# Optimization experiments

Measured on AMD Instinct MI355X. Metric: run time of the kernel, lower is better.

## Reference

```python
import jax, jax.numpy as jnp
import numpy as np

N_NODES = 100000
N_EDGES = 1600000
FEAT = 64
HEADS = 8
OUT_C = 8  # per-head out channels; HEADS*OUT_C == FEAT
BATCH = 64
MAXLEN = 2048
NEG_SLOPE = 0.2  # PyG GATConv default


def setup_inputs() -> dict:
    key = jax.random.key(0)
    ks = jax.random.split(key, 8)
    x = jax.random.normal(ks[0], (N_NODES, FEAT), dtype=jnp.float32)
    edge_index = jax.random.randint(ks[1], (2, N_EDGES), 0, N_NODES, dtype=jnp.int64)
    traj_seqs = jax.random.randint(ks[2], (BATCH, MAXLEN), 0, N_NODES, dtype=jnp.int64)
    seq_lengths = jax.random.randint(ks[3], (BATCH,), 1, MAXLEN, dtype=jnp.int64)
    # GATConv parameters (glorot-ish init)
    W = jax.random.normal(ks[4], (FEAT, HEADS * OUT_C), dtype=jnp.float32) * (1.0 / np.sqrt(FEAT))
    att_src = jax.random.normal(ks[5], (HEADS, OUT_C), dtype=jnp.float32) * 0.1
    att_dst = jax.random.normal(ks[6], (HEADS, OUT_C), dtype=jnp.float32) * 0.1
    bias = jnp.zeros((HEADS * OUT_C,), dtype=jnp.float32)
    return {"x": x, "W": W, "att_src": att_src, "att_dst": att_dst, "bias": bias,
            "edge_index": edge_index, "traj_seqs": traj_seqs, "seq_lengths": seq_lengths}


def reference(x, W, att_src, att_dst, bias, edge_index, traj_seqs, seq_lengths):
    N = x.shape[0]
    # PyG GATConv adds self loops by default
    loop = jnp.arange(N, dtype=edge_index.dtype)
    src = jnp.concatenate([edge_index[0], loop])  # message source j
    dst = jnp.concatenate([edge_index[1], loop])  # message target i

    xw = (x @ W).reshape(N, HEADS, OUT_C)              # [N,H,C]
    a_src = jnp.sum(xw * att_src, axis=-1)             # [N,H]
    a_dst = jnp.sum(xw * att_dst, axis=-1)             # [N,H]

    # edge attention logits and segment softmax over incoming edges of dst
    e = jax.nn.leaky_relu(a_src[src] + a_dst[dst], NEG_SLOPE)   # [E,H]
    m = jax.ops.segment_max(e, dst, num_segments=N)             # [N,H]
    m = jnp.where(jnp.isfinite(m), m, 0.0)
    ex = jnp.exp(e - m[dst])
    denom = jax.ops.segment_sum(ex, dst, num_segments=N)        # [N,H] (>0 via self loops)
    alpha = ex / denom[dst]                                     # [E,H]

    msg = alpha[:, :, None] * xw[src]                           # [E,H,C]
    out = jax.ops.segment_sum(msg, dst, num_segments=N)         # [N,H,C]
    node_emb = jax.nn.relu(out.reshape(N, HEADS * OUT_C) + bias)

    # batched gather into padded [B, maxlen, F] tensor, zero past seq_lengths
    emb = node_emb[traj_seqs]                                   # [B,L,F]
    mask = jnp.arange(traj_seqs.shape[1])[None, :] < seq_lengths[:, None]
    emb = emb * mask[:, :, None].astype(emb.dtype)
    return emb, seq_lengths
```

## Files before the change

### kernel.cpp

```cpp
#include <hip/hip_runtime.h>
#include <hip/hip_bf16.h>
#include <hip/hip_fp8.h>
#include <hip/hip_fp16.h>

#define N_NODESC 100000
#define N_EDGESC 1600000
#define FEATC 64
#define HEADSC 8
#define BATCHC 64
#define MAXLENC 2048
#define NBUCK 500
#define BSZ 200
#define HSZ 100
#define CAPH 3072
#define P3_EDGES 8192
#define K1B 782
#define HCHUNK 16
#define K2B 98

typedef float f32x2 __attribute__((ext_vector_type(2)));

__device__ __forceinline__ float b2f(unsigned short u){
  union { unsigned u; float f; } c; c.u = ((unsigned)u) << 16; return c.f;
}
__device__ __forceinline__ unsigned short f2b(float f){
  union { float f; unsigned u; } c; c.f = f;
  unsigned r = c.u + 0x7fffu + ((c.u >> 16) & 1u);
  return (unsigned short)(r >> 16);
}
__device__ __forceinline__ int clampi(int v, int lo, int hi){
  return v < lo ? lo : (v > hi ? hi : v);
}
__device__ __forceinline__ void unpack8(uint4 v, float* o){
  o[0] = b2f((unsigned short)(v.x & 0xffff)); o[1] = b2f((unsigned short)(v.x >> 16));
  o[2] = b2f((unsigned short)(v.y & 0xffff)); o[3] = b2f((unsigned short)(v.y >> 16));
  o[4] = b2f((unsigned short)(v.z & 0xffff)); o[5] = b2f((unsigned short)(v.z >> 16));
  o[6] = b2f((unsigned short)(v.w & 0xffff)); o[7] = b2f((unsigned short)(v.w >> 16));
}
__device__ __forceinline__ void cvt4(unsigned v, float* o){
  f32x2 lo = __builtin_amdgcn_cvt_pk_f32_fp8((int)v, false);
  f32x2 hi = __builtin_amdgcn_cvt_pk_f32_fp8((int)v, true);
  o[0] = lo.x; o[1] = lo.y; o[2] = hi.x; o[3] = hi.y;
}

__global__ __launch_bounds__(256) void k_pre(
    const unsigned short* __restrict__ x, const unsigned short* __restrict__ W,
    const unsigned short* __restrict__ attS, const unsigned short* __restrict__ attD,
    const int* __restrict__ ei,
    unsigned char* __restrict__ xw8, __half* __restrict__ a_srch,
    float* __restrict__ a_dst, int* __restrict__ cc)
{
  __shared__ unsigned short Wh[64 * 64];
  __shared__ float as_s[64];
  __shared__ float ad_s[64];
  __shared__ uint4 xs_s[128 * 9];
  __shared__ int hh[NBUCK];
  int t = threadIdx.x;

  if (blockIdx.x >= K1B) {
    for (int i = t; i < NBUCK; i += 256) hh[i] = 0;
    __syncthreads();
    int base4 = (blockIdx.x - K1B) * (HCHUNK * 256);
    #pragma unroll 4
    for (int it = 0; it < HCHUNK; it++) {
      int g = base4 + it * 256 + t;
      if (g < N_EDGESC / 4) {
        int4 d = ((const int4*)(ei + N_EDGESC))[g];
        atomicAdd(&hh[clampi(d.x, 0, N_NODESC - 1) / BSZ], 1);
        atomicAdd(&hh[clampi(d.y, 0, N_NODESC - 1) / BSZ], 1);
        atomicAdd(&hh[clampi(d.z, 0, N_NODESC - 1) / BSZ], 1);
        atomicAdd(&hh[clampi(d.w, 0, N_NODESC - 1) / BSZ], 1);
      }
    }
    __syncthreads();
    for (int i = t; i < NBUCK; i += 256) if (hh[i]) atomicAdd(&cc[i], hh[i]);
    return;
  }

  {
    const uint4* W4 = (const uint4*)W;
    ((uint4*)Wh)[t]       = W4[t];
    ((uint4*)Wh)[t + 256] = W4[t + 256];
  }
  if (t < 64) { as_s[t] = b2f(attS[t]); ad_s[t] = b2f(attD[t]); }
  {
    const uint4* x4 = (const uint4*)x;
    int gbase = blockIdx.x * 1024;
    #pragma unroll
    for (int r = 0; r < 4; r++) {
      int idx = t + r * 256;
      int nl = idx >> 3, i = idx & 7;
      uint4 v = make_uint4(0u, 0u, 0u, 0u);
      int gi = gbase + idx;
      if (gi < N_NODESC * 8) v = x4[gi];
      xs_s[nl * 9 + i] = v;
    }
  }
  __syncthreads();

  int g    = t & 3;
  int slot = t >> 2;
  int ln0  = slot * 2;
  int n0   = blockIdx.x * 128 + ln0;

  float acc[2][16];
  #pragma unroll
  for (int j = 0; j < 2; j++)
    #pragma unroll
    for (int c = 0; c < 16; c++) acc[j][c] = 0.f;

  const uint4* Wq = (const uint4*)Wh;
  for (int i = 0; i < 8; i++) {
    float xu[2][8];
    #pragma unroll
    for (int j = 0; j < 2; j++) unpack8(xs_s[(ln0 + j) * 9 + i], xu[j]);
    #pragma unroll
    for (int u = 0; u < 8; u++) {
      int k = i * 8 + u;
      float wf[16];
      unpack8(Wq[k * 8 + g * 2 + 0], wf);
      unpack8(Wq[k * 8 + g * 2 + 1], wf + 8);
      #pragma unroll
      for (int j = 0; j < 2; j++) {
        float xk = xu[j][u];
        #pragma unroll
        for (int c = 0; c < 16; c++) acc[j][c] += xk * wf[c];
      }
    }
  }

  #pragma unroll
  for (int j = 0; j < 2; j++) {
    int n = n0 + j;
    if (n >= N_NODESC) break;
    union { unsigned u[4]; unsigned char b[16]; } pk;
    #pragma unroll
    for (int c = 0; c < 16; c++)
      pk.b[c] = (unsigned char)__hip_fp8_e4m3(acc[j][c]).__x;
    uint4 o; o.x = pk.u[0]; o.y = pk.u[1]; o.z = pk.u[2]; o.w = pk.u[3];
    *((uint4*)(xw8 + (size_t)n * 64 + g * 16)) = o;

    #pragma unroll
    for (int hl = 0; hl < 2; hl++) {
      int h = g * 2 + hl;
      float sa = 0.f, sd = 0.f;
      #pragma unroll
      for (int c = 0; c < 8; c++) {
        sa += acc[j][hl * 8 + c] * as_s[h * 8 + c];
        sd += acc[j][hl * 8 + c] * ad_s[h * 8 + c];
      }
      a_srch[n * 8 + h] = __float2half(sa);
      a_dst[n * 8 + h] = sd;
    }
  }
}

__global__ __launch_bounds__(1024) void k_csort(const int* __restrict__ ei,
                                                const int* __restrict__ cc,
                                                int* __restrict__ gcur,
                                                unsigned* __restrict__ cs,
                                                int* __restrict__ boff) {
  __shared__ int bst[512];
  __shared__ int h[NBUCK], lst[NBUCK], lcur[NBUCK], gb[NBUCK];
  __shared__ int sc[512];
  __shared__ unsigned sorted[P3_EDGES];
  __shared__ unsigned short sbk[P3_EDGES];
  int t = threadIdx.x;
  int base = blockIdx.x * P3_EDGES;
  for (int i = t; i < NBUCK; i += 1024) h[i] = 0;
  int myc = 0;
  if (t < 512) { myc = (t < NBUCK) ? cc[t] : 0; bst[t] = myc; }
  __syncthreads();
  for (int off = 1; off < 512; off <<= 1) {
    int v = 0;
    if (t < 512) { v = bst[t]; if (t >= off) v += bst[t - off]; }
    __syncthreads();
    if (t < 512) bst[t] = v;
    __syncthreads();
  }
  if (blockIdx.x == 0 && t < NBUCK) boff[t] = bst[t] - myc;
  unsigned pk[8]; int bk[8];
  #pragma unroll
  for (int k = 0; k < 8; k++) {
    int idx = base + k * 1024 + t;
    bk[k] = -1;
    if (idx < N_EDGESC) {
      int s = clampi(ei[idx], 0, N_NODESC - 1);
      int d = clampi(ei[N_EDGESC + idx], 0, N_NODESC - 1);
      int b = d / BSZ;
      pk[k] = (unsigned)s | ((unsigned)(d - b * BSZ) << 17);
      bk[k] = b;
      atomicAdd(&h[b], 1);
    }
  }
  __syncthreads();
  if (t < 512) sc[t] = (t < NBUCK) ? h[t] : 0;
  __syncthreads();
  for (int off = 1; off < 512; off <<= 1) {
    int v = 0;
    if (t < 512) { v = sc[t]; if (t >= off) v += sc[t - off]; }
    __syncthreads();
    if (t < 512) sc[t] = v;
    __syncthreads();
  }
  if (t < NBUCK) {
    int ex = sc[t] - h[t];
    lst[t] = ex; lcur[t] = ex;
    if (h[t]) gb[t] = (bst[t] - myc) + atomicAdd(&gcur[t], h[t]);
  }
  __syncthreads();
  #pragma unroll
  for (int k = 0; k < 8; k++) if (bk[k] >= 0) {
    int p = atomicAdd(&lcur[bk[k]], 1);
    sorted[p] = pk[k];
    sbk[p] = (unsigned short)bk[k];
  }
  __syncthreads();
  int cnt = N_EDGESC - base; if (cnt > P3_EDGES) cnt = P3_EDGES;
  #pragma unroll
  for (int k = 0; k < 8; k++) {
    int i = k * 1024 + t;
    if (i < cnt) {
      int b = sbk[i];
      cs[gb[b] + (i - lst[b])] = sorted[i];
    }
  }
}

__global__ __launch_bounds__(512) void k_aggf(
    const __half* __restrict__ a_srch, const float* __restrict__ a_dst,
    const unsigned char* __restrict__ xw8, const unsigned* __restrict__ cs,
    const int* __restrict__ cc, const int* __restrict__ boff,
    const unsigned short* __restrict__ bias, unsigned short* __restrict__ nembh)
{
  __shared__ int lcnt[128], loff[128], lcur[128];
  __shared__ int ssrc[CAPH];
  int t = threadIdx.x;
  int b = blockIdx.x >> 1;
  int dlo = (blockIdx.x & 1) * HSZ;
  int base = boff[b];
  int cnt  = cc[b];
  if (cnt > 12 * 512) cnt = 12 * 512;

  if (t < 128) lcnt[t] = 0;
  __syncthreads();

  unsigned ce[12];
  #pragma unroll
  for (int j = 0; j < 12; j++) {
    int i = t + j * 512;
    ce[j] = 0xFFFFFFFFu;
    if (i < cnt) {
      unsigned e = cs[base + i];
      int dl = (int)(e >> 17);
      if (dl >= dlo && dl < dlo + HSZ) {
        ce[j] = e;
        atomicAdd(&lcnt[dl - dlo], 1);
      }
    }
  }
  __syncthreads();
  if (t < 128) loff[t] = lcnt[t];
  __syncthreads();
  for (int off = 1; off < 128; off <<= 1) {
    int v = 0;
    if (t < 128) { v = loff[t]; if (t >= off) v += loff[t - off]; }
    __syncthreads();
    if (t < 128) loff[t] = v;
    __syncthreads();
  }
  if (t < 128) { int ex = loff[t] - lcnt[t]; loff[t] = ex; lcur[t] = ex; }
  __syncthreads();
  #pragma unroll
  for (int j = 0; j < 12; j++) if (ce[j] != 0xFFFFFFFFu) {
    int p = atomicAdd(&lcur[(int)(ce[j] >> 17) - dlo], 1);
    if (p < CAPH) ssrc[p] = (int)(ce[j] & 0x1FFFFu);
  }
  __syncthreads();

  int wv = t >> 6;
  int l  = t & 63;
  int s  = l >> 2;
  int q  = l & 3;
  int d2 = s * 8 + wv;

  if (d2 < HSZ) {
    int dst = b * BSZ + dlo + d2;

    float2 sa2 = __half22float2(*(const __half2*)(a_srch + dst * 8 + q * 2));
    float2 ad2 = *(const float2*)(a_dst + dst * 8 + q * 2);
    float z0 = sa2.x + ad2.x, z1 = sa2.y + ad2.y;
    float den0 = __expf(fmaxf(z0, 0.2f * z0));
    float den1 = __expf(fmaxf(z1, 0.2f * z1));

    uint4 xs = *(const uint4*)(xw8 + (size_t)dst * 64 + q * 16);
    float xv[16];
    cvt4(xs.x, xv); cvt4(xs.y, xv + 4); cvt4(xs.z, xv + 8); cvt4(xs.w, xv + 12);
    float acc[16];
    #pragma unroll
    for (int c = 0; c < 8; c++) { acc[c] = den0 * xv[c]; acc[8 + c] = den1 * xv[8 + c]; }

    int beg = loff[d2]; if (beg > CAPH) beg = CAPH;
    int end2 = beg + lcnt[d2]; if (end2 > CAPH) end2 = CAPH;

    int nA = (beg < end2) ? ssrc[beg] : 0;
    int nB = (beg + 1 < end2) ? ssrc[beg + 1] : 0;
    __half2 aA = *(const __half2*)(a_srch + nA * 8 + q * 2);
    uint4   xA = *(const uint4*)(xw8 + (size_t)nA * 64 + q * 16);
    __half2 aB = *(const __half2*)(a_srch + nB * 8 + q * 2);
    uint4   xB = *(const uint4*)(xw8 + (size_t)nB * 64 + q * 16);

    for (int i = beg; i < end2; i++) {
      float2 af = __half22float2(aA);
      uint4  xc = xA;
      aA = aB; xA = xB;
      int nn = (i + 2 < end2) ? ssrc[i + 2] : 0;
      aB = *(const __half2*)(a_srch + nn * 8 + q * 2);
      xB = *(const uint4*)(xw8 + (size_t)nn * 64 + q * 16);

      float e0 = af.x + ad2.x, e1 = af.y + ad2.y;
      float w0 = __expf(fmaxf(e0, 0.2f * e0));
      float w1 = __expf(fmaxf(e1, 0.2f * e1));
      den0 += w0; den1 += w1;
      float yv[16];
      cvt4(xc.x, yv); cvt4(xc.y, yv + 4); cvt4(xc.z, yv + 8); cvt4(xc.w, yv + 12);
      #pragma unroll
      for (int c = 0; c < 8; c++) { acc[c] += w0 * yv[c]; acc[8 + c] += w1 * yv[8 + c]; }
    }

    float inv0 = __builtin_amdgcn_rcpf(den0);
    float inv1 = __builtin_amdgcn_rcpf(den1);
    uint4 bb0 = ((const uint4*)bias)[q * 2];
    uint4 bb1 = ((const uint4*)bias)[q * 2 + 1];
    unsigned bw[8] = {bb0.x, bb0.y, bb0.z, bb0.w, bb1.x, bb1.y, bb1.z, bb1.w};
    unsigned ow[8];
    #pragma unroll
    for (int p = 0; p < 8; p++) {
      float inv = (p < 4) ? inv0 : inv1;
      float v0 = acc[p * 2]     * inv + b2f((unsigned short)(bw[p] & 0xffff));
      float v1 = acc[p * 2 + 1] * inv + b2f((unsigned short)(bw[p] >> 16));
      v0 = fmaxf(v0, 0.f); v1 = fmaxf(v1, 0.f);
      ow[p] = (unsigned)f2b(v0) | ((unsigned)f2b(v1) << 16);
    }
    uint4 o0 = make_uint4(ow[0], ow[1], ow[2], ow[3]);
    uint4 o1 = make_uint4(ow[4], ow[5], ow[6], ow[7]);
    ((uint4*)nembh)[(size_t)dst * 8 + q * 2]     = o0;
    ((uint4*)nembh)[(size_t)dst * 8 + q * 2 + 1] = o1;
  }
}

__global__ __launch_bounds__(256) void k6_gather(
    const unsigned short* __restrict__ nembh, const int* __restrict__ traj,
    const int* __restrict__ lens, float* __restrict__ out)
{
  int gid = blockIdx.x * 256 + threadIdx.x;
  if (gid < BATCHC * MAXLENC * 16) {
    int b = gid >> 15;
    int rem = gid & 32767;
    int l = rem >> 4;
    int ch = rem & 15;
    int len = clampi(lens[b], 0, MAXLENC);
    float4 val = make_float4(0.f, 0.f, 0.f, 0.f);
    if (l < len) {
      int node = clampi(traj[b * MAXLENC + l], 0, N_NODESC - 1);
      uint2 q = ((const uint2*)nembh)[(size_t)node * 16 + ch];
      val = make_float4(b2f((unsigned short)(q.x & 0xffff)),
                        b2f((unsigned short)(q.x >> 16)),
                        b2f((unsigned short)(q.y & 0xffff)),
                        b2f((unsigned short)(q.y >> 16)));
    }
    ((float4*)out)[gid] = val;
  }
  if (gid < BATCHC) {
    out[(size_t)BATCHC * MAXLENC * FEATC + gid] = (float)lens[gid];
  }
}

extern "C" void kernel_launch(void* const* d_in, const int* in_sizes, int n_in,
                              void* d_out, int out_size, void* d_ws, size_t ws_size,
                              hipStream_t stream) {
  const unsigned short* x    = (const unsigned short*)d_in[0];
  const unsigned short* W    = (const unsigned short*)d_in[1];
  const unsigned short* attS = (const unsigned short*)d_in[2];
  const unsigned short* attD = (const unsigned short*)d_in[3];
  const unsigned short* bias = (const unsigned short*)d_in[4];
  const int* ei   = (const int*)d_in[5];
  const int* traj = (const int*)d_in[6];
  const int* lens = (const int*)d_in[7];
  float* out = (float*)d_out;

  float* F = (float*)d_ws;
  unsigned char* xw8 = (unsigned char*)d_ws;
  __half* a_srch = (__half*)(F + 3200000);
  float* a_dst   = F + 4000000;
  int* ccounts   = (int*)(F + 4900000);
  int* gcur      = (int*)(F + 4900000) + 512;
  int* boff      = (int*)(F + 4900000) + 1024;
  unsigned* cs   = (unsigned*)(F + 5000000);
  unsigned short* nembh = (unsigned short*)(F + 6700000);

  hipMemsetAsync(ccounts, 0, 1024 * sizeof(int), stream);
  k_pre<<<K1B + K2B, 256, 0, stream>>>(
      x, W, attS, attD, ei, xw8, a_srch, a_dst, ccounts);
  k_csort<<<(N_EDGESC + P3_EDGES - 1) / P3_EDGES, 1024, 0, stream>>>(ei, ccounts, gcur, cs, boff);
  k_aggf<<<NBUCK * 2, 512, 0, stream>>>(a_srch, a_dst, xw8, cs, ccounts, boff, bias, nembh);
  k6_gather<<<(BATCHC * MAXLENC * 16 + 255) / 256, 256, 0, stream>>>(nembh, traj, lens, out);
}
```

Baseline: 171.4 us.

## Halve per-thread nodes in projection and scatter edges directly in bucket sort

```diff
diff --git a/kernel.cpp b/kernel.cpp
--- a/kernel.cpp
+++ b/kernel.cpp
@@ -13,10 +13,11 @@
 #define BSZ 200
 #define HSZ 100
 #define CAPH 3072
-#define P3_EDGES 8192
-#define K1B 782
+#define K1B 1563
 #define HCHUNK 16
 #define K2B 98
+#define CS_EPB 4096
+#define CSB 391
 
 typedef float f32x2 __attribute__((ext_vector_type(2)));
 
@@ -53,7 +54,7 @@
   __shared__ unsigned short Wh[64 * 64];
   __shared__ float as_s[64];
   __shared__ float ad_s[64];
-  __shared__ uint4 xs_s[128 * 9];
+  __shared__ uint4 xs_s[64 * 9];
   __shared__ int hh[NBUCK];
   int t = threadIdx.x;
 
@@ -85,9 +86,9 @@
   if (t < 64) { as_s[t] = b2f(attS[t]); ad_s[t] = b2f(attD[t]); }
   {
     const uint4* x4 = (const uint4*)x;
-    int gbase = blockIdx.x * 1024;
-    #pragma unroll
-    for (int r = 0; r < 4; r++) {
+    int gbase = blockIdx.x * 512;
+    #pragma unroll
+    for (int r = 0; r < 2; r++) {
       int idx = t + r * 256;
       int nl = idx >> 3, i = idx & 7;
       uint4 v = make_uint4(0u, 0u, 0u, 0u);
@@ -100,43 +101,33 @@
 
   int g    = t & 3;
   int slot = t >> 2;
-  int ln0  = slot * 2;
-  int n0   = blockIdx.x * 128 + ln0;
-
-  float acc[2][16];
-  #pragma unroll
-  for (int j = 0; j < 2; j++)
-    #pragma unroll
-    for (int c = 0; c < 16; c++) acc[j][c] = 0.f;
+  int n    = blockIdx.x * 64 + slot;
+
+  float acc[16];
+  #pragma unroll
+  for (int c = 0; c < 16; c++) acc[c] = 0.f;
 
   const uint4* Wq = (const uint4*)Wh;
   for (int i = 0; i < 8; i++) {
-    float xu[2][8];
-    #pragma unroll
-    for (int j = 0; j < 2; j++) unpack8(xs_s[(ln0 + j) * 9 + i], xu[j]);
+    float xu[8];
+    unpack8(xs_s[slot * 9 + i], xu);
     #pragma unroll
     for (int u = 0; u < 8; u++) {
       int k = i * 8 + u;
       float wf[16];
       unpack8(Wq[k * 8 + g * 2 + 0], wf);
       unpack8(Wq[k * 8 + g * 2 + 1], wf + 8);
+      float xk = xu[u];
       #pragma unroll
-      for (int j = 0; j < 2; j++) {
-        float xk = xu[j][u];
-        #pragma unroll
-        for (int c = 0; c < 16; c++) acc[j][c] += xk * wf[c];
-      }
-    }
-  }
-
-  #pragma unroll
-  for (int j = 0; j < 2; j++) {
-    int n = n0 + j;
-    if (n >= N_NODESC) break;
+      for (int c = 0; c < 16; c++) acc[c] += xk * wf[c];
+    }
+  }
+
+  if (n < N_NODESC) {
     union { unsigned u[4]; unsigned char b[16]; } pk;
     #pragma unroll
     for (int c = 0; c < 16; c++)
-      pk.b[c] = (unsigned char)__hip_fp8_e4m3(acc[j][c]).__x;
+      pk.b[c] = (unsigned char)__hip_fp8_e4m3(acc[c]).__x;
     uint4 o; o.x = pk.u[0]; o.y = pk.u[1]; o.z = pk.u[2]; o.w = pk.u[3];
     *((uint4*)(xw8 + (size_t)n * 64 + g * 16)) = o;
 
@@ -146,8 +137,8 @@
       float sa = 0.f, sd = 0.f;
       #pragma unroll
       for (int c = 0; c < 8; c++) {
-        sa += acc[j][hl * 8 + c] * as_s[h * 8 + c];
-        sd += acc[j][hl * 8 + c] * ad_s[h * 8 + c];
+        sa += acc[hl * 8 + c] * as_s[h * 8 + c];
+        sd += acc[hl * 8 + c] * ad_s[h * 8 + c];
       }
       a_srch[n * 8 + h] = __float2half(sa);
       a_dst[n * 8 + h] = sd;
@@ -155,34 +146,33 @@
   }
 }
 
-__global__ __launch_bounds__(1024) void k_csort(const int* __restrict__ ei,
-                                                const int* __restrict__ cc,
-                                                int* __restrict__ gcur,
-                                                unsigned* __restrict__ cs,
-                                                int* __restrict__ boff) {
+__global__ __launch_bounds__(512) void k_csort(const int* __restrict__ ei,
+                                               const int* __restrict__ cc,
+                                               int* __restrict__ gcur,
+                                               unsigned* __restrict__ cs,
+                                               int* __restrict__ boff) {
   __shared__ int bst[512];
-  __shared__ int h[NBUCK], lst[NBUCK], lcur[NBUCK], gb[NBUCK];
-  __shared__ int sc[512];
-  __shared__ unsigned sorted[P3_EDGES];
-  __shared__ unsigned short sbk[P3_EDGES];
+  __shared__ int h[NBUCK];
+  __shared__ int lcur[NBUCK];
   int t = threadIdx.x;
-  int base = blockIdx.x * P3_EDGES;
-  for (int i = t; i < NBUCK; i += 1024) h[i] = 0;
-  int myc = 0;
-  if (t < 512) { myc = (t < NBUCK) ? cc[t] : 0; bst[t] = myc; }
+  int base = blockIdx.x * CS_EPB;
+  for (int i = t; i < NBUCK; i += 512) h[i] = 0;
+  int myc = (t < NBUCK) ? cc[t] : 0;
+  bst[t] = myc;
   __syncthreads();
   for (int off = 1; off < 512; off <<= 1) {
-    int v = 0;
-    if (t < 512) { v = bst[t]; if (t >= off) v += bst[t - off]; }
-    __syncthreads();
-    if (t < 512) bst[t] = v;
+    int v = bst[t];
+    if (t >= off) v += bst[t - off];
+    __syncthreads();
+    bst[t] = v;
     __syncthreads();
   }
   if (blockIdx.x == 0 && t < NBUCK) boff[t] = bst[t] - myc;
+
   unsigned pk[8]; int bk[8];
   #pragma unroll
   for (int k = 0; k < 8; k++) {
-    int idx = base + k * 1024 + t;
+    int idx = base + k * 512 + t;
     bk[k] = -1;
     if (idx < N_EDGESC) {
       int s = clampi(ei[idx], 0, N_NODESC - 1);
@@ -194,36 +184,13 @@
     }
   }
   __syncthreads();
-  if (t < 512) sc[t] = (t < NBUCK) ? h[t] : 0;
-  __syncthreads();
-  for (int off = 1; off < 512; off <<= 1) {
-    int v = 0;
-    if (t < 512) { v = sc[t]; if (t >= off) v += sc[t - off]; }
-    __syncthreads();
-    if (t < 512) sc[t] = v;
-    __syncthreads();
-  }
-  if (t < NBUCK) {
-    int ex = sc[t] - h[t];
-    lst[t] = ex; lcur[t] = ex;
-    if (h[t]) gb[t] = (bst[t] - myc) + atomicAdd(&gcur[t], h[t]);
-  }
+  if (t < NBUCK && h[t])
+    lcur[t] = (bst[t] - myc) + atomicAdd(&gcur[t], h[t]);
   __syncthreads();
   #pragma unroll
   for (int k = 0; k < 8; k++) if (bk[k] >= 0) {
     int p = atomicAdd(&lcur[bk[k]], 1);
-    sorted[p] = pk[k];
-    sbk[p] = (unsigned short)bk[k];
-  }
-  __syncthreads();
-  int cnt = N_EDGESC - base; if (cnt > P3_EDGES) cnt = P3_EDGES;
-  #pragma unroll
-  for (int k = 0; k < 8; k++) {
-    int i = k * 1024 + t;
-    if (i < cnt) {
-      int b = sbk[i];
-      cs[gb[b] + (i - lst[b])] = sorted[i];
-    }
+    cs[p] = pk[k];
   }
 }
 
@@ -402,7 +369,7 @@
   hipMemsetAsync(ccounts, 0, 1024 * sizeof(int), stream);
   k_pre<<<K1B + K2B, 256, 0, stream>>>(
       x, W, attS, attD, ei, xw8, a_srch, a_dst, ccounts);
-  k_csort<<<(N_EDGESC + P3_EDGES - 1) / P3_EDGES, 1024, 0, stream>>>(ei, ccounts, gcur, cs, boff);
+  k_csort<<<CSB, 512, 0, stream>>>(ei, ccounts, gcur, cs, boff);
   k_aggf<<<NBUCK * 2, 512, 0, stream>>>(a_srch, a_dst, xw8, cs, ccounts, boff, bias, nembh);
   k6_gather<<<(BATCHC * MAXLENC * 16 + 255) / 256, 256, 0, stream>>>(nembh, traj, lens, out);
 }
```

New measurement: 181.2 us. 5.7% more time.
